# Kernel optimization log

Measured on AMD Instinct MI355X. Metric: run time of the kernel, lower is better.

Reference implementation:

```python
import jax, jax.numpy as jnp
import numpy as np

QMAX = 127.0  # int8 symmetric range


def fake_quant(t):
    """Per-tensor symmetric int8 quantize->dequantize (HMQ-style numerics)."""
    scale = jnp.maximum(jnp.max(jnp.abs(t)), 1e-8) / QMAX
    q = jnp.clip(jnp.round(t / scale), -QMAX, QMAX)
    return q * scale


def hmq_linear(x, w, b):
    # quantize activations and weights, dequantized GEMM + bias
    xq = fake_quant(x)
    wq = fake_quant(w)
    return jnp.einsum('bsi,oi->bso', xq, wq) + b


def setup_inputs() -> dict:
    key = jax.random.key(0)
    k = jax.random.split(key, 5)
    d, h = 1024, 4096
    return {
        'x': jax.random.normal(k[0], (4, 4096, d), dtype=jnp.float32),
        'w1': jax.random.normal(k[1], (h, d), dtype=jnp.float32) * 0.02,
        'b1': jax.random.normal(k[2], (h,), dtype=jnp.float32) * 0.02,
        'w2': jax.random.normal(k[3], (d, h), dtype=jnp.float32) * 0.02,
        'b2': jax.random.normal(k[4], (d,), dtype=jnp.float32) * 0.02,
    }


def reference(x, w1, b1, w2, b2):
    h = hmq_linear(x, w1, b1)          # fc1 (quantized)
    h = jax.nn.gelu(h, approximate=False)  # HMQGeLU (exact erf GELU)
    out = hmq_linear(h, w2, b2)        # fc2 (quantized)
    return out
```

## Files before the change

### kernel.cpp

```cpp
#include <hip/hip_runtime.h>
#include <hip/hip_bf16.h>
#include <math.h>
#include <stdint.h>


typedef int    v4i    __attribute__((ext_vector_type(4)));
typedef short  short8 __attribute__((ext_vector_type(8)));
typedef int8_t char8  __attribute__((ext_vector_type(8)));

#define QMAXF 127.0f

__device__ __forceinline__ float gelu_exact(float v) {
    float z = fabsf(v) * 0.70710678118654752440f;
    float t = __builtin_amdgcn_rcpf(fmaf(0.3275911f, z, 1.0f));
    float p = fmaf(fmaf(fmaf(fmaf(1.061405429f, t, -1.453152027f), t,
                             1.421413741f), t, -0.284496736f), t,
                   0.254829592f) * t;
    float e = __expf(-z * z);
    float erfz = fmaf(-p, e, 1.0f);
    float erfv = v < 0.f ? -erfz : erfz;
    return 0.5f * v * (1.0f + erfv);
}

__global__ void init_slots(unsigned int* slots) {
    if (threadIdx.x < 8) slots[threadIdx.x] = 0u;
}

__global__ void absmax_kernel(const float4* __restrict__ t, int n4,
                              unsigned int* __restrict__ slot) {
    float m = 0.f;
    int stride = gridDim.x * blockDim.x;
    for (int i = blockIdx.x * blockDim.x + threadIdx.x; i < n4; i += stride) {
        float4 v = t[i];
        m = fmaxf(m, fmaxf(fmaxf(fabsf(v.x), fabsf(v.y)),
                           fmaxf(fabsf(v.z), fabsf(v.w))));
    }
#pragma unroll
    for (int off = 32; off > 0; off >>= 1)
        m = fmaxf(m, __shfl_xor(m, off));
    if ((threadIdx.x & 63) == 0)
        atomicMax(slot, __float_as_uint(m));
}

__global__ void quant_stage_kernel(const float* __restrict__ x, int kshift,
                                   int nblocks, const float* __restrict__ slot,
                                   int8_t* __restrict__ q) {
    const float s = fmaxf(*slot, 1e-8f) / QMAXF;
    const int lane = threadIdx.x & 63;
    const int wave0 = (blockIdx.x * blockDim.x + threadIdx.x) >> 6;
    const int nwaves = (gridDim.x * blockDim.x) >> 6;
    const int nkb = 1 << kshift;
    for (int wb = wave0; wb < nblocks; wb += nwaves) {
        const int rb = wb >> kshift;
        const int kc = wb & (nkb - 1);
        const int row = rb * 16 + (lane & 15);
        const int k0  = kc * 64 + (lane >> 4) * 16;
        const float4* src = (const float4*)(x + ((size_t)row << (kshift + 6)) + k0);
        int8_t tmp[16];
#pragma unroll
        for (int j = 0; j < 4; j++) {
            float4 v = src[j];
            tmp[j*4+0] = (int8_t)fminf(fmaxf(rintf(v.x / s), -127.f), 127.f);
            tmp[j*4+1] = (int8_t)fminf(fmaxf(rintf(v.y / s), -127.f), 127.f);
            tmp[j*4+2] = (int8_t)fminf(fmaxf(rintf(v.z / s), -127.f), 127.f);
            tmp[j*4+3] = (int8_t)fminf(fmaxf(rintf(v.w / s), -127.f), 127.f);
        }
        *(int4*)(q + (size_t)wb * 1024 + lane * 16) = *(const int4*)tmp;
    }
}

__global__ void quant_h_kernel(const short8* __restrict__ h16s,
                               const float* __restrict__ tilescale,
                               const float* __restrict__ hslot,
                               char8* __restrict__ q, int n8) {
    const float sh = fmaxf(*hslot, 1e-8f) / QMAXF;
    int stride = gridDim.x * blockDim.x;
    for (int i = blockIdx.x * blockDim.x + threadIdx.x; i < n8; i += stride) {
        const int blk = i >> 7;
        const int rb = blk >> 6, kc = blk & 63;
        const int tile = (rb >> 3) * 32 + (kc >> 1);
        const float f = tilescale[tile] / (32767.f * sh);
        short8 v = h16s[i];
        char8 o;
#pragma unroll
        for (int j = 0; j < 8; j++)
            o[j] = (int8_t)fminf(fmaxf(rintf((float)v[j] * f), -127.f), 127.f);
        q[i] = o;
    }
}

#define EPI_G1_STORE_I16 0
#define EPI_G1_MAXONLY   1
#define EPI_G1_QUANT     2
#define EPI_G2_OUT       3

template <int EPI>
__global__ __launch_bounds__(256, 3) void gemm_i8_kernel(
    const int8_t* __restrict__ A, const int8_t* __restrict__ B,
    int N, int K,
    const float* __restrict__ slotA, const float* __restrict__ slotB,
    const float* __restrict__ bias,
    int16_t* __restrict__ h16_out,
    float* __restrict__ tilescale,
    unsigned int* __restrict__ maxslot,
    const float* __restrict__ hslot,
    int8_t* __restrict__ q_out,
    float* __restrict__ out)
{
    __shared__ __align__(16) int16_t tl[16384];
    __shared__ float red[4];

    const int tid  = threadIdx.x;
    const int lane = tid & 63;
    const int wv   = tid >> 6;
    const int wm   = wv & 1;
    const int wn   = wv >> 1;

    const int bm = blockIdx.x * 128;
    const int bn = blockIdx.y * 128;
    const int nkb = K >> 6;

    const float sAB = (fmaxf(*slotA, 1e-8f) / QMAXF) *
                      (fmaxf(*slotB, 1e-8f) / QMAXF);

    v4i acc[4][4] = {};

    const size_t rbstride = (size_t)nkb * 1024;
    const int8_t* pA = A + (size_t)((bm >> 4) + wm * 4) * rbstride + lane * 16;
    const int8_t* pB = B + (size_t)((bn >> 4) + wn * 4) * rbstride + lane * 16;

    auto loadA = [&](v4i (&d)[4], int k) {
#pragma unroll
        for (int i = 0; i < 4; i++)
            d[i] = *(const v4i*)(pA + (size_t)i * rbstride + (size_t)k * 1024);
    };
    auto loadB = [&](v4i (&d)[4], int k) {
#pragma unroll
        for (int i = 0; i < 4; i++)
            d[i] = *(const v4i*)(pB + (size_t)i * rbstride + (size_t)k * 1024);
    };
    auto mfma_all = [&](v4i (&a)[4], v4i (&b)[4]) {
#pragma unroll
        for (int mi = 0; mi < 4; mi++)
#pragma unroll
            for (int ni = 0; ni < 4; ni++)
                acc[mi][ni] = __builtin_amdgcn_mfma_i32_16x16x64_i8(
                    a[mi], b[ni], acc[mi][ni], 0, 0, 0);
    };

    v4i a0[4], b0[4], a1[4], b1[4];
    loadA(a0, 0); loadB(b0, 0);
    loadA(a1, 1); loadB(b1, 1);
    int kt = 0;
    for (; kt + 2 < nkb; kt += 2) {
        mfma_all(a0, b0);
        loadA(a0, kt + 2); loadB(b0, kt + 2);
        mfma_all(a1, b1);
        loadA(a1, kt + 3); loadB(b1, kt + 3);
    }
    mfma_all(a0, b0);
    mfma_all(a1, b1);

    float sc_q = 0.f;
    if constexpr (EPI == EPI_G1_QUANT) sc_q = fmaxf(*hslot, 1e-8f) / QMAXF;
    float lmax = 0.f;

#pragma unroll
    for (int mi = 0; mi < 4; mi++) {
#pragma unroll
        for (int ni = 0; ni < 4; ni++) {
            const int col = bn + wn * 64 + ni * 16 + (lane & 15);
            const float bv = bias[col];
#pragma unroll
            for (int r = 0; r < 4; r++) {
                float val = (float)acc[mi][ni][r] * sAB + bv;
                if constexpr (EPI == EPI_G2_OUT) {
                    acc[mi][ni][r] = __float_as_int(val);
                } else {
                    float g = gelu_exact(val);
                    lmax = fmaxf(lmax, fabsf(g));
                    acc[mi][ni][r] = __float_as_int(g);
                }
            }
        }
    }

    float enc = 0.f;
    if constexpr (EPI == EPI_G1_STORE_I16 || EPI == EPI_G1_MAXONLY) {
#pragma unroll
        for (int off = 32; off > 0; off >>= 1)
            lmax = fmaxf(lmax, __shfl_xor(lmax, off));
        if (lane == 0) red[wv] = lmax;
        __syncthreads();
        const float m = fmaxf(fmaxf(red[0], red[1]), fmaxf(red[2], red[3]));
        if (tid == 0) {
            if constexpr (EPI == EPI_G1_STORE_I16)
                tilescale[blockIdx.x * gridDim.y + blockIdx.y] = m;
            atomicMax(maxslot, __float_as_uint(m));
        }
        enc = 32767.f / fmaxf(m, 1e-20f);
    }

    if constexpr (EPI == EPI_G1_STORE_I16) {
        const int base16 = wv * 4096;
#pragma unroll
        for (int mi = 0; mi < 4; mi++)
#pragma unroll
            for (int ni = 0; ni < 4; ni++)
#pragma unroll
                for (int r = 0; r < 4; r++) {
                    float g = __int_as_float(acc[mi][ni][r]);
                    tl[base16 + mi * 1024 + ni * 256 +
                       ((lane >> 4) * 4 + r) * 16 + (lane & 15)] =
                        (int16_t)rintf(g * enc);
                }
        __syncthreads();
        const int kc = (bn >> 6) + wn;
#pragma unroll
        for (int mi = 0; mi < 4; mi++) {
            const int rb = (bm >> 4) + wm * 4 + mi;
            int16_t* dst = h16_out + ((size_t)rb * (N >> 6) + kc) * 1024;
            const int16_t* src = tl + base16 + mi * 1024;
            *(int4*)(dst + lane * 8)       = *(const int4*)(src + lane * 8);
            *(int4*)(dst + 512 + lane * 8) = *(const int4*)(src + 512 + lane * 8);
        }
    } else if constexpr (EPI != EPI_G1_MAXONLY) {
#pragma unroll
        for (int mi = 0; mi < 4; mi++) {
            const int row0 = bm + wm * 64 + mi * 16 + (lane >> 4) * 4;
#pragma unroll
            for (int ni = 0; ni < 4; ni++) {
                const int col = bn + wn * 64 + ni * 16 + (lane & 15);
#pragma unroll
                for (int r = 0; r < 4; r++) {
                    const int row = row0 + r;
                    float g = __int_as_float(acc[mi][ni][r]);
                    if constexpr (EPI == EPI_G2_OUT) {
                        out[(size_t)row * N + col] = g;
                    } else {
                        float qv = fminf(fmaxf(rintf(g / sc_q), -127.f), 127.f);
                        size_t off = ((size_t)(row >> 4) * (N >> 6) + (col >> 6)) * 1024
                                   + ((col >> 4) & 3) * 256 + (row & 15) * 16 + (col & 15);
                        q_out[off] = (int8_t)qv;
                    }
                }
            }
        }
    }
}


extern "C" void kernel_launch(void* const* d_in, const int* in_sizes, int n_in,
                              void* d_out, int out_size, void* d_ws, size_t ws_size,
                              hipStream_t stream) {
    const float* x  = (const float*)d_in[0];
    const float* w1 = (const float*)d_in[1];
    const float* b1 = (const float*)d_in[2];
    const float* w2 = (const float*)d_in[3];
    const float* b2 = (const float*)d_in[4];
    float* out = (float*)d_out;

    const int D = 1024, H = 4096;
    const int Mrows = 4 * 4096;

    uintptr_t ws = (uintptr_t)d_ws;
    unsigned int* slots = (unsigned int*)ws;
    const float* slotf = (const float*)ws;
    float* tiles = (float*)(ws + 256);
    int8_t* xq  = (int8_t*)(ws + 256 + 65536);
    int8_t* w1q = xq + (size_t)Mrows * D;
    int8_t* w2q = w1q + (size_t)H * D;
    int8_t* hq  = w2q + (size_t)D * H;
    int16_t* h16 = (int16_t*)(hq + (size_t)Mrows * H);
    const size_t need_i16 =
        256 + 65536 + (size_t)Mrows * D + 2u * (size_t)H * D +
        (size_t)Mrows * H + (size_t)Mrows * H * sizeof(int16_t);
    const bool use_store = ws_size >= need_i16;

    init_slots<<<dim3(1), dim3(64), 0, stream>>>(slots);
    absmax_kernel<<<dim3(1024), dim3(256), 0, stream>>>(
        (const float4*)x, Mrows * D / 4, slots + 0);
    absmax_kernel<<<dim3(256), dim3(256), 0, stream>>>(
        (const float4*)w1, H * D / 4, slots + 1);
    absmax_kernel<<<dim3(256), dim3(256), 0, stream>>>(
        (const float4*)w2, D * H / 4, slots + 2);

    quant_stage_kernel<<<dim3(1024), dim3(256), 0, stream>>>(
        x, 4, (Mrows / 16) * (D / 64), slotf + 0, xq);
    quant_stage_kernel<<<dim3(256), dim3(256), 0, stream>>>(
        w1, 4, (H / 16) * (D / 64), slotf + 1, w1q);
    quant_stage_kernel<<<dim3(256), dim3(256), 0, stream>>>(
        w2, 6, (D / 16) * (H / 64), slotf + 2, w2q);

    dim3 g1(Mrows / 128, H / 128);
    if (use_store) {
        gemm_i8_kernel<EPI_G1_STORE_I16><<<g1, dim3(256), 0, stream>>>(
            xq, w1q, H, D, slotf + 0, slotf + 1, b1,
            h16, tiles, slots + 3, nullptr, nullptr, nullptr);
        quant_h_kernel<<<dim3(2048), dim3(256), 0, stream>>>(
            (const short8*)h16, tiles, slotf + 3, (char8*)hq, Mrows * H / 8);
    } else {
        gemm_i8_kernel<EPI_G1_MAXONLY><<<g1, dim3(256), 0, stream>>>(
            xq, w1q, H, D, slotf + 0, slotf + 1, b1,
            nullptr, nullptr, slots + 3, nullptr, nullptr, nullptr);
        gemm_i8_kernel<EPI_G1_QUANT><<<g1, dim3(256), 0, stream>>>(
            xq, w1q, H, D, slotf + 0, slotf + 1, b1,
            nullptr, nullptr, nullptr, slotf + 3, hq, nullptr);
    }

    dim3 g2(Mrows / 128, D / 128);
    gemm_i8_kernel<EPI_G2_OUT><<<g2, dim3(256), 0, stream>>>(
        hq, w2q, D, H, slotf + 3, slotf + 2, b2,
        nullptr, nullptr, nullptr, nullptr, nullptr, out);
}
```

Measured before the change: 474.0 us.

## Widen GEMM block tile to 128x256 and coalesce quant staging through LDS

The int8 GEMM now computes a 128x256 output tile per block, with each wave holding 4x8 accumulators, so each A fragment is reused across twice as many MFMAs. Grids are halved in N and launch bounds drop to 2 blocks per CU to fit the larger register footprint. Per-tile scales are written twice so quant_h_kernel keeps its old tile indexing, at the cost of coarser int16 intermediate scaling. The quant staging kernel separately loads contiguous rows into shared memory for coalesced global reads before packing into the MFMA layout.

After: 461.7 us. -2.6%, faster.

```diff
diff --git a/kernel.cpp b/kernel.cpp
--- a/kernel.cpp
+++ b/kernel.cpp
@@ -45,25 +45,32 @@
 __global__ void quant_stage_kernel(const float* __restrict__ x, int kshift,
                                    int nblocks, const float* __restrict__ slot,
                                    int8_t* __restrict__ q) {
+    __shared__ float qt[4][1088];
     const float s = fmaxf(*slot, 1e-8f) / QMAXF;
     const int lane = threadIdx.x & 63;
+    const int wv   = threadIdx.x >> 6;
     const int wave0 = (blockIdx.x * blockDim.x + threadIdx.x) >> 6;
     const int nwaves = (gridDim.x * blockDim.x) >> 6;
     const int nkb = 1 << kshift;
+    const int K = 64 << kshift;
+    float* tw = &qt[wv][0];
     for (int wb = wave0; wb < nblocks; wb += nwaves) {
         const int rb = wb >> kshift;
         const int kc = wb & (nkb - 1);
-        const int row = rb * 16 + (lane & 15);
-        const int k0  = kc * 64 + (lane >> 4) * 16;
-        const float4* src = (const float4*)(x + ((size_t)row << (kshift + 6)) + k0);
+#pragma unroll
+        for (int j = 0; j < 4; j++) {
+            const int row = rb * 16 + j * 4 + (lane >> 4);
+            float4 v = *(const float4*)(x + (size_t)row * K + kc * 64 + (lane & 15) * 4);
+            *(float4*)(tw + (j * 4 + (lane >> 4)) * 68 + (lane & 15) * 4) = v;
+        }
         int8_t tmp[16];
 #pragma unroll
-        for (int j = 0; j < 4; j++) {
-            float4 v = src[j];
-            tmp[j*4+0] = (int8_t)fminf(fmaxf(rintf(v.x / s), -127.f), 127.f);
-            tmp[j*4+1] = (int8_t)fminf(fmaxf(rintf(v.y / s), -127.f), 127.f);
-            tmp[j*4+2] = (int8_t)fminf(fmaxf(rintf(v.z / s), -127.f), 127.f);
-            tmp[j*4+3] = (int8_t)fminf(fmaxf(rintf(v.w / s), -127.f), 127.f);
+        for (int t = 0; t < 4; t++) {
+            float4 v = *(const float4*)(tw + (lane & 15) * 68 + (lane >> 4) * 16 + t * 4);
+            tmp[t*4+0] = (int8_t)fminf(fmaxf(rintf(v.x / s), -127.f), 127.f);
+            tmp[t*4+1] = (int8_t)fminf(fmaxf(rintf(v.y / s), -127.f), 127.f);
+            tmp[t*4+2] = (int8_t)fminf(fmaxf(rintf(v.z / s), -127.f), 127.f);
+            tmp[t*4+3] = (int8_t)fminf(fmaxf(rintf(v.w / s), -127.f), 127.f);
         }
         *(int4*)(q + (size_t)wb * 1024 + lane * 16) = *(const int4*)tmp;
     }
@@ -95,7 +102,7 @@
 #define EPI_G2_OUT       3
 
 template <int EPI>
-__global__ __launch_bounds__(256, 3) void gemm_i8_kernel(
+__global__ __launch_bounds__(256, 2) void gemm_i8_kernel(
     const int8_t* __restrict__ A, const int8_t* __restrict__ B,
     int N, int K,
     const float* __restrict__ slotA, const float* __restrict__ slotB,
@@ -117,38 +124,39 @@
     const int wn   = wv >> 1;
 
     const int bm = blockIdx.x * 128;
-    const int bn = blockIdx.y * 128;
+    const int bn = blockIdx.y * 256;
     const int nkb = K >> 6;
 
     const float sAB = (fmaxf(*slotA, 1e-8f) / QMAXF) *
                       (fmaxf(*slotB, 1e-8f) / QMAXF);
 
-    v4i acc[4][4] = {};
+    v4i acc[4][8] = {};
 
     const size_t rbstride = (size_t)nkb * 1024;
     const int8_t* pA = A + (size_t)((bm >> 4) + wm * 4) * rbstride + lane * 16;
-    const int8_t* pB = B + (size_t)((bn >> 4) + wn * 4) * rbstride + lane * 16;
+    const int8_t* pB = B + (size_t)((bn >> 4) + wn * 8) * rbstride + lane * 16;
 
     auto loadA = [&](v4i (&d)[4], int k) {
 #pragma unroll
         for (int i = 0; i < 4; i++)
             d[i] = *(const v4i*)(pA + (size_t)i * rbstride + (size_t)k * 1024);
     };
-    auto loadB = [&](v4i (&d)[4], int k) {
-#pragma unroll
-        for (int i = 0; i < 4; i++)
+    auto loadB = [&](v4i (&d)[8], int k) {
+#pragma unroll
+        for (int i = 0; i < 8; i++)
             d[i] = *(const v4i*)(pB + (size_t)i * rbstride + (size_t)k * 1024);
     };
-    auto mfma_all = [&](v4i (&a)[4], v4i (&b)[4]) {
+    auto mfma_all = [&](v4i (&a)[4], v4i (&b)[8]) {
 #pragma unroll
         for (int mi = 0; mi < 4; mi++)
 #pragma unroll
-            for (int ni = 0; ni < 4; ni++)
+            for (int ni = 0; ni < 8; ni++)
                 acc[mi][ni] = __builtin_amdgcn_mfma_i32_16x16x64_i8(
                     a[mi], b[ni], acc[mi][ni], 0, 0, 0);
     };
 
-    v4i a0[4], b0[4], a1[4], b1[4];
+    v4i a0[4], a1[4];
+    v4i b0[8], b1[8];
     loadA(a0, 0); loadB(b0, 0);
     loadA(a1, 1); loadB(b1, 1);
     int kt = 0;
@@ -168,8 +176,8 @@
 #pragma unroll
     for (int mi = 0; mi < 4; mi++) {
 #pragma unroll
-        for (int ni = 0; ni < 4; ni++) {
-            const int col = bn + wn * 64 + ni * 16 + (lane & 15);
+        for (int ni = 0; ni < 8; ni++) {
+            const int col = bn + wn * 128 + ni * 16 + (lane & 15);
             const float bv = bias[col];
 #pragma unroll
             for (int r = 0; r < 4; r++) {
@@ -194,43 +202,50 @@
         __syncthreads();
         const float m = fmaxf(fmaxf(red[0], red[1]), fmaxf(red[2], red[3]));
         if (tid == 0) {
-            if constexpr (EPI == EPI_G1_STORE_I16)
-                tilescale[blockIdx.x * gridDim.y + blockIdx.y] = m;
+            if constexpr (EPI == EPI_G1_STORE_I16) {
+                const int tbase = blockIdx.x * (gridDim.y * 2) + blockIdx.y * 2;
+                tilescale[tbase]     = m;
+                tilescale[tbase + 1] = m;
+            }
             atomicMax(maxslot, __float_as_uint(m));
         }
         enc = 32767.f / fmaxf(m, 1e-20f);
     }
 
     if constexpr (EPI == EPI_G1_STORE_I16) {
-        const int base16 = wv * 4096;
-#pragma unroll
-        for (int mi = 0; mi < 4; mi++)
-#pragma unroll
-            for (int ni = 0; ni < 4; ni++)
-#pragma unroll
-                for (int r = 0; r < 4; r++) {
-                    float g = __int_as_float(acc[mi][ni][r]);
-                    tl[base16 + mi * 1024 + ni * 256 +
-                       ((lane >> 4) * 4 + r) * 16 + (lane & 15)] =
-                        (int16_t)rintf(g * enc);
+        const int r16 = (lane >> 4) * 4;
+        const int c15 = lane & 15;
+#pragma unroll
+        for (int half = 0; half < 2; half++) {
+#pragma unroll
+            for (int mi = 0; mi < 4; mi++)
+#pragma unroll
+                for (int nih = 0; nih < 4; nih++) {
+                    const int ni = half * 4 + nih;
+#pragma unroll
+                    for (int r = 0; r < 4; r++) {
+                        float g = __int_as_float(acc[mi][ni][r]);
+                        tl[wv * 4096 + mi * 1024 + nih * 256 + (r16 + r) * 16 + c15] =
+                            (int16_t)rintf(g * enc);
+                    }
                 }
-        __syncthreads();
-        const int kc = (bn >> 6) + wn;
-#pragma unroll
-        for (int mi = 0; mi < 4; mi++) {
-            const int rb = (bm >> 4) + wm * 4 + mi;
-            int16_t* dst = h16_out + ((size_t)rb * (N >> 6) + kc) * 1024;
-            const int16_t* src = tl + base16 + mi * 1024;
-            *(int4*)(dst + lane * 8)       = *(const int4*)(src + lane * 8);
-            *(int4*)(dst + 512 + lane * 8) = *(const int4*)(src + 512 + lane * 8);
+            const int kc = (bn >> 6) + wn * 2 + half;
+#pragma unroll
+            for (int mi = 0; mi < 4; mi++) {
+                const int rb = (bm >> 4) + wm * 4 + mi;
+                int16_t* dst = h16_out + ((size_t)rb * (N >> 6) + kc) * 1024;
+                const int16_t* src = tl + wv * 4096 + mi * 1024;
+                *(int4*)(dst + lane * 8)       = *(const int4*)(src + lane * 8);
+                *(int4*)(dst + 512 + lane * 8) = *(const int4*)(src + 512 + lane * 8);
+            }
         }
     } else if constexpr (EPI != EPI_G1_MAXONLY) {
 #pragma unroll
         for (int mi = 0; mi < 4; mi++) {
             const int row0 = bm + wm * 64 + mi * 16 + (lane >> 4) * 4;
 #pragma unroll
-            for (int ni = 0; ni < 4; ni++) {
-                const int col = bn + wn * 64 + ni * 16 + (lane & 15);
+            for (int ni = 0; ni < 8; ni++) {
+                const int col = bn + wn * 128 + ni * 16 + (lane & 15);
 #pragma unroll
                 for (int r = 0; r < 4; r++) {
                     const int row = row0 + r;
@@ -292,7 +307,7 @@
     quant_stage_kernel<<<dim3(256), dim3(256), 0, stream>>>(
         w2, 6, (D / 16) * (H / 64), slotf + 2, w2q);
 
-    dim3 g1(Mrows / 128, H / 128);
+    dim3 g1(Mrows / 128, H / 256);
     if (use_store) {
         gemm_i8_kernel<EPI_G1_STORE_I16><<<g1, dim3(256), 0, stream>>>(
             xq, w1q, H, D, slotf + 0, slotf + 1, b1,
@@ -308,7 +323,7 @@
             nullptr, nullptr, nullptr, slotf + 3, hq, nullptr);
     }
 
-    dim3 g2(Mrows / 128, D / 128);
+    dim3 g2(Mrows / 128, D / 256);
     gemm_i8_kernel<EPI_G2_OUT><<<g2, dim3(256), 0, stream>>>(
         hq, w2q, D, H, slotf + 3, slotf + 2, b2,
         nullptr, nullptr, nullptr, nullptr, nullptr, out);
```
